# Optimization experiments

Measured on AMD Instinct MI355X. Metric: run time of the kernel, lower is better.

Reference implementation:

```python
import jax, jax.numpy as jnp
import numpy as np

B, T, N = 64, 1024, 1024  # n = 2*hidden_size

def setup_inputs() -> dict:
    key = jax.random.key(0)
    ks = jax.random.split(key, 8)
    s = 1.0 / np.sqrt(N)
    return {
        "s_t_hat": jax.random.normal(ks[0], (B, N), jnp.float32),
        "h": jax.random.normal(ks[1], (B, T, N), jnp.float32),
        "enc_padding_mask": jnp.ones((B, T), jnp.float32),
        "coverage": jax.random.uniform(ks[2], (B, T), jnp.float32),
        "W_h": jax.random.normal(ks[3], (N, N), jnp.float32) * s,   # Linear(N,N,bias=False), [out,in]
        "W_c": jax.random.normal(ks[4], (N,), jnp.float32) * s,     # Linear(1,N,bias=False) weight[:,0]
        "dec_W": jax.random.normal(ks[5], (N, N), jnp.float32) * s, # decode_proj weight [out,in]
        "dec_b": jax.random.normal(ks[6], (N,), jnp.float32) * s,   # decode_proj bias
        "v": jax.random.normal(ks[7], (N,), jnp.float32) * s,       # Linear(N,1,bias=False) weight[0,:]
    }

def reference(s_t_hat, h, enc_padding_mask, coverage, W_h, W_c, dec_W, dec_b, v):
    # encoder_feature = W_h(h): [B,T,N]
    enc_feat = jnp.einsum("btn,mn->btm", h, W_h)
    # dec_fea = decode_proj(s_t_hat): [B,N], broadcast over T
    dec_fea = s_t_hat @ dec_W.T + dec_b
    att = enc_feat + dec_fea[:, None, :]
    # coverage feature: coverage[...,None] * W_c row (Linear(1,N))
    att = att + coverage[:, :, None] * W_c[None, None, :]
    # scores = v(tanh(att)): [B,T]
    scores = jnp.einsum("btn,n->bt", jnp.tanh(att), v)
    attn_ = jax.nn.softmax(scores, axis=1) * enc_padding_mask
    attn = attn_ / jnp.sum(attn_, axis=1, keepdims=True)
    # context vector: [B,N]
    c_t = jnp.einsum("bt,btn->bn", attn, h)
    coverage_new = coverage + attn
    return (c_t, attn, coverage_new)
```

## Files before the change

kernel.cpp:

```cpp
#include <hip/hip_runtime.h>

typedef __bf16 bf16x8 __attribute__((ext_vector_type(8)));
typedef float f32x4 __attribute__((ext_vector_type(4)));
typedef unsigned short us8 __attribute__((ext_vector_type(8)));

#define B_ 64
#define T_ 1024
#define N_ 1024

__device__ __forceinline__ unsigned short f2bf(float f) {
  unsigned int u = __float_as_uint(f);
  u += 0x7fffu + ((u >> 16) & 1u);
  return (unsigned short)(u >> 16);
}

__device__ __forceinline__ float fast_tanh(float x) {
  float xc = fminf(fmaxf(x, -15.f), 15.f);
  float e = __expf(2.f * xc);
  return (e - 1.f) / (e + 1.f);
}

__device__ __forceinline__ void async16(const unsigned short* g, unsigned short* l) {
  __builtin_amdgcn_global_load_lds((const __attribute__((address_space(1))) void*)g,
                                   (__attribute__((address_space(3))) void*)l, 16, 0, 0);
}

__global__ __launch_bounds__(256) void k_cvt_wh(const float* __restrict__ W_h,
                                                unsigned short* __restrict__ whb,
                                                float* __restrict__ scores,
                                                float* __restrict__ ct) {
  int base = blockIdx.x * 256 + threadIdx.x;
  size_t i = (size_t)base * 4;
  float4 x = *(const float4*)(W_h + i);
  ushort4 o;
  o.x = f2bf(x.x); o.y = f2bf(x.y); o.z = f2bf(x.z); o.w = f2bf(x.w);
  *(ushort4*)(whb + i) = o;
  if (base < B_ * T_) scores[base] = 0.f;
  if (base < B_ * N_) ct[base] = 0.f;
}

__global__ __launch_bounds__(256) void k_cvt_h(const float* __restrict__ h,
                                               unsigned short* __restrict__ hbf) {
  size_t i = ((size_t)blockIdx.x * 256 + threadIdx.x) * 8;
  float4 x = *(const float4*)(h + i);
  float4 y = *(const float4*)(h + i + 4);
  us8 o;
  o[0] = f2bf(x.x); o[1] = f2bf(x.y); o[2] = f2bf(x.z); o[3] = f2bf(x.w);
  o[4] = f2bf(y.x); o[5] = f2bf(y.y); o[6] = f2bf(y.z); o[7] = f2bf(y.w);
  *(us8*)(hbf + i) = o;
}

__global__ __launch_bounds__(256) void k_decfea2(const float* __restrict__ s_t_hat,
                                                 const float* __restrict__ dec_W,
                                                 const float* __restrict__ dec_b,
                                                 float* __restrict__ dec_fea) {
  const int m0 = blockIdx.x * 64;
  const int bg0 = blockIdx.y * 8;
  __shared__ float sh[8][N_];
  __shared__ float red[4][64][8];
  const int tid = threadIdx.x;
  for (int idx = tid; idx < 8 * N_; idx += 256) {
    int bb = idx >> 10, k = idx & (N_ - 1);
    sh[bb][k] = s_t_hat[(size_t)(bg0 + bb) * N_ + k];
  }
  __syncthreads();
  const int tm = tid >> 2;
  const int seg = tid & 3;
  const float* w = dec_W + (size_t)(m0 + tm) * N_;
  float acc[8];
#pragma unroll
  for (int bb = 0; bb < 8; bb++) acc[bb] = 0.f;
  for (int i = 0; i < 64; i++) {
    int k = seg * 4 + i * 16;
    float4 wv = *(const float4*)(w + k);
#pragma unroll
    for (int bb = 0; bb < 8; bb++)
      acc[bb] += sh[bb][k] * wv.x + sh[bb][k + 1] * wv.y + sh[bb][k + 2] * wv.z + sh[bb][k + 3] * wv.w;
  }
#pragma unroll
  for (int bb = 0; bb < 8; bb++) red[seg][tm][bb] = acc[bb];
  __syncthreads();
  int om = tid & 63, ob = tid >> 6;
#pragma unroll
  for (int p = 0; p < 2; p++) {
    int obb = ob + p * 4;
    float s = red[0][om][obb] + red[1][om][obb] + red[2][om][obb] + red[3][om][obb] + dec_b[m0 + om];
    dec_fea[(size_t)(bg0 + obb) * N_ + m0 + om] = s;
  }
}

__global__ __launch_bounds__(256) void k_score2(
    const unsigned short* __restrict__ hbf, const unsigned short* __restrict__ whb,
    const float* __restrict__ dec_fea, const float* __restrict__ coverage,
    const float* __restrict__ W_c, const float* __restrict__ v,
    float* __restrict__ scores) {
  __shared__ __align__(16) unsigned short lsA[128 * 32];
  __shared__ __align__(16) unsigned short lsB[128 * 32];

  const int tid = threadIdx.x;
  const int bid = blockIdx.x;
  const int xcd = bid & 7;
  const int local = bid >> 3;
  const int mi = local & 7;
  const int tb = xcd * 64 + (local >> 3);
  const int b = tb >> 3;
  const int t0 = (tb & 7) * 128;
  const int m0 = mi * 128;

  const int wave = tid >> 6, lane = tid & 63;
  const int wr = wave >> 1, wc = wave & 1;
  const int lm = lane & 15, lq = lane >> 4;

  f32x4 acc[4][4];
#pragma unroll
  for (int i = 0; i < 4; i++)
#pragma unroll
    for (int j = 0; j < 4; j++) acc[i][j] = (f32x4){0.f, 0.f, 0.f, 0.f};

  const int r0 = tid >> 2;
  const int key0 = (r0 & 3) ^ ((r0 >> 2) & 3);
  const int cc = ((tid & 3) ^ key0) * 8;
  const unsigned short* gA = hbf + ((size_t)(b * T_ + t0)) * N_;
  const unsigned short* gB = whb + (size_t)m0 * N_;
  const size_t ga0 = (size_t)r0 * N_ + cc;
  const size_t ga1 = (size_t)(r0 + 64) * N_ + cc;
  unsigned short* la0 = &lsA[tid * 8];
  unsigned short* la1 = &lsA[(tid + 256) * 8];
  unsigned short* lb0 = &lsB[tid * 8];
  unsigned short* lb1 = &lsB[(tid + 256) * 8];

  const int keyL = (lm & 3) ^ ((lm >> 2) & 3);
  const int rdoff = (lq ^ keyL) * 8;

  for (int k0 = 0; k0 < N_; k0 += 32) {
    async16(gA + ga0 + k0, la0);
    async16(gA + ga1 + k0, la1);
    async16(gB + ga0 + k0, lb0);
    async16(gB + ga1 + k0, lb1);
    __syncthreads();

    bf16x8 af[4], bfr[4];
#pragma unroll
    for (int i = 0; i < 4; i++)
      af[i] = __builtin_bit_cast(bf16x8, *(const us8*)&lsA[(wr * 64 + i * 16 + lm) * 32 + rdoff]);
#pragma unroll
    for (int j = 0; j < 4; j++)
      bfr[j] = __builtin_bit_cast(bf16x8, *(const us8*)&lsB[(wc * 64 + j * 16 + lm) * 32 + rdoff]);
#pragma unroll
    for (int i = 0; i < 4; i++)
#pragma unroll
      for (int j = 0; j < 4; j++)
        acc[i][j] = __builtin_amdgcn_mfma_f32_16x16x32_bf16(af[i], bfr[j], acc[i][j], 0, 0, 0);
    __syncthreads();
  }

  float dfv[4], wcv[4], vv[4];
#pragma unroll
  for (int j = 0; j < 4; j++) {
    int m = m0 + wc * 64 + j * 16 + lm;
    dfv[j] = dec_fea[b * N_ + m];
    wcv[j] = W_c[m];
    vv[j] = v[m];
  }
#pragma unroll
  for (int i = 0; i < 4; i++) {
#pragma unroll
    for (int r = 0; r < 4; r++) {
      int t = t0 + wr * 64 + i * 16 + lq * 4 + r;
      float cv = coverage[b * T_ + t];
      float s = 0.f;
#pragma unroll
      for (int j = 0; j < 4; j++) {
        float x = acc[i][j][r] + dfv[j] + cv * wcv[j];
        s += fast_tanh(x) * vv[j];
      }
      s += __shfl_xor(s, 1);
      s += __shfl_xor(s, 2);
      s += __shfl_xor(s, 4);
      s += __shfl_xor(s, 8);
      if (lm == 0) atomicAdd(&scores[b * T_ + t], s);
    }
  }
}

__global__ __launch_bounds__(256) void k_score_fb(
    const float* __restrict__ h, const unsigned short* __restrict__ whb,
    const float* __restrict__ dec_fea, const float* __restrict__ coverage,
    const float* __restrict__ W_c, const float* __restrict__ v,
    float* __restrict__ scores) {
  __shared__ __align__(16) unsigned short lsA[128 * 40];
  __shared__ __align__(16) unsigned short lsB[128 * 40];
  const int tid = threadIdx.x;
  const int b = blockIdx.z;
  const int t0 = blockIdx.y * 128;
  const int m0 = blockIdx.x * 128;
  const int wave = tid >> 6, lane = tid & 63;
  const int wr = wave >> 1, wc = wave & 1;
  const int lm = lane & 15, lq = lane >> 4;
  f32x4 acc[4][4];
#pragma unroll
  for (int i = 0; i < 4; i++)
#pragma unroll
    for (int j = 0; j < 4; j++) acc[i][j] = (f32x4){0.f, 0.f, 0.f, 0.f};
  const float* hA = h + ((size_t)b * T_ + t0) * N_;
  const unsigned short* wB = whb + (size_t)m0 * N_;
  for (int k0 = 0; k0 < N_; k0 += 32) {
    __syncthreads();
    for (int s = tid; s < 512; s += 256) {
      int row = s >> 2, kc = (s & 3) * 8;
      const float* src = hA + (size_t)row * N_ + k0 + kc;
      float4 x = *(const float4*)src;
      float4 y = *(const float4*)(src + 4);
      unsigned short* d = &lsA[row * 40 + kc];
      d[0] = f2bf(x.x); d[1] = f2bf(x.y); d[2] = f2bf(x.z); d[3] = f2bf(x.w);
      d[4] = f2bf(y.x); d[5] = f2bf(y.y); d[6] = f2bf(y.z); d[7] = f2bf(y.w);
    }
    for (int s = tid; s < 512; s += 256) {
      int row = s >> 2, kc = (s & 3) * 8;
      us8 x = *(const us8*)(wB + (size_t)row * N_ + k0 + kc);
      *(us8*)&lsB[row * 40 + kc] = x;
    }
    __syncthreads();
    bf16x8 af[4], bfr[4];
#pragma unroll
    for (int i = 0; i < 4; i++)
      af[i] = __builtin_bit_cast(bf16x8, *(const us8*)&lsA[(wr * 64 + i * 16 + lm) * 40 + lq * 8]);
#pragma unroll
    for (int j = 0; j < 4; j++)
      bfr[j] = __builtin_bit_cast(bf16x8, *(const us8*)&lsB[(wc * 64 + j * 16 + lm) * 40 + lq * 8]);
#pragma unroll
    for (int i = 0; i < 4; i++)
#pragma unroll
      for (int j = 0; j < 4; j++)
        acc[i][j] = __builtin_amdgcn_mfma_f32_16x16x32_bf16(af[i], bfr[j], acc[i][j], 0, 0, 0);
  }
  float dfv[4], wcv[4], vv[4];
#pragma unroll
  for (int j = 0; j < 4; j++) {
    int m = m0 + wc * 64 + j * 16 + lm;
    dfv[j] = dec_fea[b * N_ + m];
    wcv[j] = W_c[m];
    vv[j] = v[m];
  }
#pragma unroll
  for (int i = 0; i < 4; i++) {
#pragma unroll
    for (int r = 0; r < 4; r++) {
      int t = t0 + wr * 64 + i * 16 + lq * 4 + r;
      float cv = coverage[b * T_ + t];
      float s = 0.f;
#pragma unroll
      for (int j = 0; j < 4; j++) {
        float x = acc[i][j][r] + dfv[j] + cv * wcv[j];
        s += fast_tanh(x) * vv[j];
      }
      s += __shfl_xor(s, 1);
      s += __shfl_xor(s, 2);
      s += __shfl_xor(s, 4);
      s += __shfl_xor(s, 8);
      if (lm == 0) atomicAdd(&scores[b * T_ + t], s);
    }
  }
}

__global__ __launch_bounds__(256) void k_softmax(const float* __restrict__ scores,
                                                 const float* __restrict__ mask,
                                                 const float* __restrict__ coverage,
                                                 float* __restrict__ attn_out,
                                                 float* __restrict__ cov_out) {
  const int b = blockIdx.x, tid = threadIdx.x;
  const int wave = tid >> 6, lane = tid & 63;
  const float* s = scores + b * T_;
  float vals[4];
  float lmax = -1e30f;
#pragma unroll
  for (int i = 0; i < 4; i++) {
    vals[i] = s[i * 256 + tid];
    lmax = fmaxf(lmax, vals[i]);
  }
#pragma unroll
  for (int off = 1; off < 64; off <<= 1) lmax = fmaxf(lmax, __shfl_xor(lmax, off));
  __shared__ float rmax[4], rsum[4];
  if (lane == 0) rmax[wave] = lmax;
  __syncthreads();
  float bmax = fmaxf(fmaxf(rmax[0], rmax[1]), fmaxf(rmax[2], rmax[3]));
  float w[4];
  float lsum = 0.f;
#pragma unroll
  for (int i = 0; i < 4; i++) {
    float e = __expf(vals[i] - bmax) * mask[b * T_ + i * 256 + tid];
    w[i] = e;
    lsum += e;
  }
#pragma unroll
  for (int off = 1; off < 64; off <<= 1) lsum += __shfl_xor(lsum, off);
  if (lane == 0) rsum[wave] = lsum;
  __syncthreads();
  float inv = 1.f / (rsum[0] + rsum[1] + rsum[2] + rsum[3]);
#pragma unroll
  for (int i = 0; i < 4; i++) {
    int t = i * 256 + tid;
    float a = w[i] * inv;
    attn_out[b * T_ + t] = a;
    cov_out[b * T_ + t] = coverage[b * T_ + t] + a;
  }
}

__global__ __launch_bounds__(256) void k_ctx2(const unsigned short* __restrict__ hbf,
                                              const float* __restrict__ attn,
                                              float* __restrict__ c_t) {
  const int b = blockIdx.y;
  const int t0 = blockIdx.x * 128;
  const int tid = threadIdx.x;
  const int n0 = (tid & 127) * 8;
  const int tp = tid >> 7;
  __shared__ float la[128];
  __shared__ float part[128][8];
  if (tid < 128) la[tid] = attn[b * T_ + t0 + tid];
  __syncthreads();
  float acc[8] = {0.f, 0.f, 0.f, 0.f, 0.f, 0.f, 0.f, 0.f};
  for (int t = tp; t < 128; t += 2) {
    const uint4 u = *(const uint4*)(hbf + ((size_t)(b * T_ + t0 + t)) * N_ + n0);
    float a = la[t];
    acc[0] += a * __uint_as_float(u.x << 16);
    acc[1] += a * __uint_as_float(u.x & 0xffff0000u);
    acc[2] += a * __uint_as_float(u.y << 16);
    acc[3] += a * __uint_as_float(u.y & 0xffff0000u);
    acc[4] += a * __uint_as_float(u.z << 16);
    acc[5] += a * __uint_as_float(u.z & 0xffff0000u);
    acc[6] += a * __uint_as_float(u.w << 16);
    acc[7] += a * __uint_as_float(u.w & 0xffff0000u);
  }
  if (tp == 1) {
#pragma unroll
    for (int j = 0; j < 8; j++) part[tid & 127][j] = acc[j];
  }
  __syncthreads();
  if (tp == 0) {
#pragma unroll
    for (int j = 0; j < 8; j++)
      atomicAdd(&c_t[b * N_ + n0 + j], acc[j] + part[tid][j]);
  }
}

__global__ __launch_bounds__(256) void k_ctx_fb(const float* __restrict__ h,
                                                const float* __restrict__ attn,
                                                float* __restrict__ c_t) {
  const int b = blockIdx.y;
  const int n = blockIdx.x * 256 + threadIdx.x;
  __shared__ float la[T_];
  for (int i = threadIdx.x; i < T_; i += 256) la[i] = attn[b * T_ + i];
  __syncthreads();
  const float* hb = h + (size_t)b * T_ * N_ + n;
  float acc = 0.f;
#pragma unroll 8
  for (int t = 0; t < T_; t++) acc += la[t] * hb[(size_t)t * N_];
  c_t[b * N_ + n] = acc;
}

extern "C" void kernel_launch(void* const* d_in, const int* in_sizes, int n_in,
                              void* d_out, int out_size, void* d_ws, size_t ws_size,
                              hipStream_t stream) {
  const float* s_t_hat  = (const float*)d_in[0];
  const float* h        = (const float*)d_in[1];
  const float* mask     = (const float*)d_in[2];
  const float* coverage = (const float*)d_in[3];
  const float* W_h      = (const float*)d_in[4];
  const float* W_c      = (const float*)d_in[5];
  const float* dec_W    = (const float*)d_in[6];
  const float* dec_b    = (const float*)d_in[7];
  const float* v        = (const float*)d_in[8];

  float* out = (float*)d_out;
  float* out_ct   = out;
  float* out_attn = out + B_ * T_;
  float* out_cov  = out + 2 * B_ * T_;

  const size_t hbf_bytes = (size_t)B_ * T_ * N_ * 2;
  const size_t whb_bytes = (size_t)N_ * N_ * 2;
  const size_t df_bytes  = (size_t)B_ * N_ * 4;
  const size_t sc_bytes  = (size_t)B_ * T_ * 4;
  const bool big = ws_size >= hbf_bytes + whb_bytes + df_bytes + sc_bytes;

  char* ws = (char*)d_ws;
  if (big) {
    unsigned short* hbf = (unsigned short*)ws;
    unsigned short* whb = (unsigned short*)(ws + hbf_bytes);
    float* dec_fea = (float*)(ws + hbf_bytes + whb_bytes);
    float* scores  = (float*)(ws + hbf_bytes + whb_bytes + df_bytes);

    k_cvt_wh<<<dim3(N_ * N_ / 1024), 256, 0, stream>>>(W_h, whb, scores, out_ct);
    k_cvt_h<<<dim3(B_ * T_ * N_ / 2048), 256, 0, stream>>>(h, hbf);
    k_decfea2<<<dim3(16, 8), 256, 0, stream>>>(s_t_hat, dec_W, dec_b, dec_fea);
    k_score2<<<dim3(4096), 256, 0, stream>>>(hbf, whb, dec_fea, coverage, W_c, v, scores);
    k_softmax<<<dim3(B_), 256, 0, stream>>>(scores, mask, coverage, out_attn, out_cov);
    k_ctx2<<<dim3(T_ / 128, B_), 256, 0, stream>>>(hbf, out_attn, out_ct);
  } else {
    unsigned short* whb = (unsigned short*)ws;
    float* dec_fea = (float*)(ws + whb_bytes);
    float* scores  = (float*)(ws + whb_bytes + df_bytes);

    k_cvt_wh<<<dim3(N_ * N_ / 1024), 256, 0, stream>>>(W_h, whb, scores, out_ct);
    k_decfea2<<<dim3(16, 8), 256, 0, stream>>>(s_t_hat, dec_W, dec_b, dec_fea);
    k_score_fb<<<dim3(N_ / 128, T_ / 128, B_), 256, 0, stream>>>(h, whb, dec_fea, coverage, W_c, v, scores);
    k_softmax<<<dim3(B_), 256, 0, stream>>>(scores, mask, coverage, out_attn, out_cov);
    k_ctx_fb<<<dim3(4, B_), 256, 0, stream>>>(h, out_attn, out_ct);
  }
}
```

Measured before the change: 672.0 us.

## Pre-swizzle h and W_h into MFMA fragment layout, drop LDS staging

The bf16 conversion kernels now write h and W_h in a tiled layout where each 16x32 tile is stored in the exact per-lane order the MFMA fragment expects. The score GEMM then loads fragments straight from global memory into registers with double buffering, removing the LDS async copies and the two barriers per k-step. The context kernel is rewritten to read the same swizzled layout, reducing across lanes with shuffles before the atomics. The risk is that tiles in a block are no longer reused through LDS, so the GEMM leans on L2 for reuse and global load latency is less well hidden.

```diff
diff --git a/kernel.cpp b/kernel.cpp
--- a/kernel.cpp
+++ b/kernel.cpp
@@ -20,34 +20,44 @@
   return (e - 1.f) / (e + 1.f);
 }
 
-__device__ __forceinline__ void async16(const unsigned short* g, unsigned short* l) {
-  __builtin_amdgcn_global_load_lds((const __attribute__((address_space(1))) void*)g,
-                                   (__attribute__((address_space(3))) void*)l, 16, 0, 0);
-}
-
-__global__ __launch_bounds__(256) void k_cvt_wh(const float* __restrict__ W_h,
-                                                unsigned short* __restrict__ whb,
-                                                float* __restrict__ scores,
-                                                float* __restrict__ ct) {
-  int base = blockIdx.x * 256 + threadIdx.x;
-  size_t i = (size_t)base * 4;
-  float4 x = *(const float4*)(W_h + i);
-  ushort4 o;
-  o.x = f2bf(x.x); o.y = f2bf(x.y); o.z = f2bf(x.z); o.w = f2bf(x.w);
-  *(ushort4*)(whb + i) = o;
-  if (base < B_ * T_) scores[base] = 0.f;
-  if (base < B_ * N_) ct[base] = 0.f;
-}
-
-__global__ __launch_bounds__(256) void k_cvt_h(const float* __restrict__ h,
-                                               unsigned short* __restrict__ hbf) {
-  size_t i = ((size_t)blockIdx.x * 256 + threadIdx.x) * 8;
-  float4 x = *(const float4*)(h + i);
-  float4 y = *(const float4*)(h + i + 4);
+
+__global__ __launch_bounds__(256) void k_swz_w(const float* __restrict__ W_h,
+                                               unsigned short* __restrict__ wsw,
+                                               float* __restrict__ scores,
+                                               float* __restrict__ ct) {
+  const int tau = blockIdx.x * 4 + (threadIdx.x >> 6);
+  const int l = threadIdx.x & 63;
+  const int mb = tau >> 5, kb = tau & 31;
+  const int row = mb * 16 + (l & 15);
+  const int kof = kb * 32 + (l >> 4) * 8;
+  const float* src = W_h + (size_t)row * N_ + kof;
+  float4 x = *(const float4*)src;
+  float4 y = *(const float4*)(src + 4);
   us8 o;
   o[0] = f2bf(x.x); o[1] = f2bf(x.y); o[2] = f2bf(x.z); o[3] = f2bf(x.w);
   o[4] = f2bf(y.x); o[5] = f2bf(y.y); o[6] = f2bf(y.z); o[7] = f2bf(y.w);
-  *(us8*)(hbf + i) = o;
+  *(us8*)(wsw + (size_t)tau * 512 + l * 8) = o;
+  const int gid = blockIdx.x * 256 + threadIdx.x;
+  if (gid < B_ * T_) scores[gid] = 0.f;
+  if (gid < B_ * N_) ct[gid] = 0.f;
+}
+
+__global__ __launch_bounds__(256) void k_swz_h(const float* __restrict__ h,
+                                               unsigned short* __restrict__ hs) {
+  const int tau = blockIdx.x * 4 + (threadIdx.x >> 6);
+  const int l = threadIdx.x & 63;
+  const int b = tau >> 11;
+  const int tb = (tau >> 5) & 63;
+  const int kb = tau & 31;
+  const int row = tb * 16 + (l & 15);
+  const int kof = kb * 32 + (l >> 4) * 8;
+  const float* src = h + ((size_t)(b << 10) + row) * N_ + kof;
+  float4 x = *(const float4*)src;
+  float4 y = *(const float4*)(src + 4);
+  us8 o;
+  o[0] = f2bf(x.x); o[1] = f2bf(x.y); o[2] = f2bf(x.z); o[3] = f2bf(x.w);
+  o[4] = f2bf(y.x); o[5] = f2bf(y.y); o[6] = f2bf(y.z); o[7] = f2bf(y.w);
+  *(us8*)(hs + (size_t)tau * 512 + l * 8) = o;
 }
 
 __global__ __launch_bounds__(256) void k_decfea2(const float* __restrict__ s_t_hat,
@@ -89,14 +99,11 @@
   }
 }
 
-__global__ __launch_bounds__(256) void k_score2(
-    const unsigned short* __restrict__ hbf, const unsigned short* __restrict__ whb,
+__global__ __launch_bounds__(256) void k_score3(
+    const unsigned short* __restrict__ hs, const unsigned short* __restrict__ wsw,
     const float* __restrict__ dec_fea, const float* __restrict__ coverage,
     const float* __restrict__ W_c, const float* __restrict__ v,
     float* __restrict__ scores) {
-  __shared__ __align__(16) unsigned short lsA[128 * 32];
-  __shared__ __align__(16) unsigned short lsB[128 * 32];
-
   const int tid = threadIdx.x;
   const int bid = blockIdx.x;
   const int xcd = bid & 7;
@@ -104,8 +111,9 @@
   const int mi = local & 7;
   const int tb = xcd * 64 + (local >> 3);
   const int b = tb >> 3;
-  const int t0 = (tb & 7) * 128;
+  const int t8 = tb & 7;
   const int m0 = mi * 128;
+  const int t0 = t8 * 128;
 
   const int wave = tid >> 6, lane = tid & 63;
   const int wr = wave >> 1, wc = wave & 1;
@@ -117,41 +125,42 @@
 #pragma unroll
     for (int j = 0; j < 4; j++) acc[i][j] = (f32x4){0.f, 0.f, 0.f, 0.f};
 
-  const int r0 = tid >> 2;
-  const int key0 = (r0 & 3) ^ ((r0 >> 2) & 3);
-  const int cc = ((tid & 3) ^ key0) * 8;
-  const unsigned short* gA = hbf + ((size_t)(b * T_ + t0)) * N_;
-  const unsigned short* gB = whb + (size_t)m0 * N_;
-  const size_t ga0 = (size_t)r0 * N_ + cc;
-  const size_t ga1 = (size_t)(r0 + 64) * N_ + cc;
-  unsigned short* la0 = &lsA[tid * 8];
-  unsigned short* la1 = &lsA[(tid + 256) * 8];
-  unsigned short* lb0 = &lsB[tid * 8];
-  unsigned short* lb1 = &lsB[(tid + 256) * 8];
-
-  const int keyL = (lm & 3) ^ ((lm >> 2) & 3);
-  const int rdoff = (lq ^ keyL) * 8;
-
-  for (int k0 = 0; k0 < N_; k0 += 32) {
-    async16(gA + ga0 + k0, la0);
-    async16(gA + ga1 + k0, la1);
-    async16(gB + ga0 + k0, lb0);
-    async16(gB + ga1 + k0, lb1);
-    __syncthreads();
-
-    bf16x8 af[4], bfr[4];
+  const unsigned short* pA = hs + (((size_t)b * 64 + t8 * 8 + wr * 4) << 5 << 9) + lane * 8;
+  const unsigned short* pB = wsw + (((size_t)(mi * 8 + wc * 4)) << 5 << 9) + lane * 8;
+
+  us8 aA[4], bA[4], aB[4], bB[4];
+#pragma unroll
+  for (int i = 0; i < 4; i++) {
+    aA[i] = *(const us8*)(pA + ((i << 5) << 9));
+    bA[i] = *(const us8*)(pB + ((i << 5) << 9));
+  }
+  for (int kb = 0; kb < 32; kb += 2) {
+#pragma unroll
+    for (int i = 0; i < 4; i++) {
+      aB[i] = *(const us8*)(pA + (((i << 5) + kb + 1) << 9));
+      bB[i] = *(const us8*)(pB + (((i << 5) + kb + 1) << 9));
+    }
 #pragma unroll
     for (int i = 0; i < 4; i++)
-      af[i] = __builtin_bit_cast(bf16x8, *(const us8*)&lsA[(wr * 64 + i * 16 + lm) * 32 + rdoff]);
-#pragma unroll
-    for (int j = 0; j < 4; j++)
-      bfr[j] = __builtin_bit_cast(bf16x8, *(const us8*)&lsB[(wc * 64 + j * 16 + lm) * 32 + rdoff]);
+#pragma unroll
+      for (int j = 0; j < 4; j++)
+        acc[i][j] = __builtin_amdgcn_mfma_f32_16x16x32_bf16(
+            __builtin_bit_cast(bf16x8, aA[i]), __builtin_bit_cast(bf16x8, bA[j]),
+            acc[i][j], 0, 0, 0);
+    if (kb + 2 < 32) {
+#pragma unroll
+      for (int i = 0; i < 4; i++) {
+        aA[i] = *(const us8*)(pA + (((i << 5) + kb + 2) << 9));
+        bA[i] = *(const us8*)(pB + (((i << 5) + kb + 2) << 9));
+      }
+    }
 #pragma unroll
     for (int i = 0; i < 4; i++)
 #pragma unroll
       for (int j = 0; j < 4; j++)
-        acc[i][j] = __builtin_amdgcn_mfma_f32_16x16x32_bf16(af[i], bfr[j], acc[i][j], 0, 0, 0);
-    __syncthreads();
+        acc[i][j] = __builtin_amdgcn_mfma_f32_16x16x32_bf16(
+            __builtin_bit_cast(bf16x8, aB[i]), __builtin_bit_cast(bf16x8, bB[j]),
+            acc[i][j], 0, 0, 0);
   }
 
   float dfv[4], wcv[4], vv[4];
@@ -263,6 +272,20 @@
   }
 }
 
+__global__ __launch_bounds__(256) void k_cvt_wh(const float* __restrict__ W_h,
+                                                unsigned short* __restrict__ whb,
+                                                float* __restrict__ scores,
+                                                float* __restrict__ ct) {
+  int base = blockIdx.x * 256 + threadIdx.x;
+  size_t i = (size_t)base * 4;
+  float4 x = *(const float4*)(W_h + i);
+  ushort4 o;
+  o.x = f2bf(x.x); o.y = f2bf(x.y); o.z = f2bf(x.z); o.w = f2bf(x.w);
+  *(ushort4*)(whb + i) = o;
+  if (base < B_ * T_) scores[base] = 0.f;
+  if (base < B_ * N_) ct[base] = 0.f;
+}
+
 __global__ __launch_bounds__(256) void k_softmax(const float* __restrict__ scores,
                                                  const float* __restrict__ mask,
                                                  const float* __restrict__ coverage,
@@ -306,40 +329,37 @@
   }
 }
 
-__global__ __launch_bounds__(256) void k_ctx2(const unsigned short* __restrict__ hbf,
+__global__ __launch_bounds__(256) void k_ctx3(const unsigned short* __restrict__ hs,
                                               const float* __restrict__ attn,
                                               float* __restrict__ c_t) {
   const int b = blockIdx.y;
-  const int t0 = blockIdx.x * 128;
-  const int tid = threadIdx.x;
-  const int n0 = (tid & 127) * 8;
-  const int tp = tid >> 7;
-  __shared__ float la[128];
-  __shared__ float part[128][8];
-  if (tid < 128) la[tid] = attn[b * T_ + t0 + tid];
-  __syncthreads();
+  const int z = blockIdx.z;
+  const int kb = blockIdx.x * 4 + (threadIdx.x >> 6);
+  const int l = threadIdx.x & 63;
+  __shared__ float la[T_];
+  for (int i = threadIdx.x; i < T_; i += 256) la[i] = attn[b * T_ + i];
+  __syncthreads();
+  const unsigned short* p = hs + (((size_t)b * 64 + z * 32) << 5 << 9) + ((size_t)kb << 9) + l * 8;
   float acc[8] = {0.f, 0.f, 0.f, 0.f, 0.f, 0.f, 0.f, 0.f};
-  for (int t = tp; t < 128; t += 2) {
-    const uint4 u = *(const uint4*)(hbf + ((size_t)(b * T_ + t0 + t)) * N_ + n0);
-    float a = la[t];
-    acc[0] += a * __uint_as_float(u.x << 16);
-    acc[1] += a * __uint_as_float(u.x & 0xffff0000u);
-    acc[2] += a * __uint_as_float(u.y << 16);
-    acc[3] += a * __uint_as_float(u.y & 0xffff0000u);
-    acc[4] += a * __uint_as_float(u.z << 16);
-    acc[5] += a * __uint_as_float(u.z & 0xffff0000u);
-    acc[6] += a * __uint_as_float(u.w << 16);
-    acc[7] += a * __uint_as_float(u.w & 0xffff0000u);
-  }
-  if (tp == 1) {
-#pragma unroll
-    for (int j = 0; j < 8; j++) part[tid & 127][j] = acc[j];
-  }
-  __syncthreads();
-  if (tp == 0) {
-#pragma unroll
-    for (int j = 0; j < 8; j++)
-      atomicAdd(&c_t[b * N_ + n0 + j], acc[j] + part[tid][j]);
+  const int trow = l & 15;
+#pragma unroll 4
+  for (int tb = 0; tb < 32; tb++) {
+    us8 u = *(const us8*)(p + ((size_t)tb << 5 << 9));
+    float a = la[(z * 32 + tb) * 16 + trow];
+#pragma unroll
+    for (int j = 0; j < 8; j++) acc[j] += a * __uint_as_float((unsigned)u[j] << 16);
+  }
+#pragma unroll
+  for (int j = 0; j < 8; j++) {
+    acc[j] += __shfl_xor(acc[j], 1);
+    acc[j] += __shfl_xor(acc[j], 2);
+    acc[j] += __shfl_xor(acc[j], 4);
+    acc[j] += __shfl_xor(acc[j], 8);
+  }
+  if (trow == 0) {
+    int n0 = kb * 32 + (l >> 4) * 8;
+#pragma unroll
+    for (int j = 0; j < 8; j++) atomicAdd(&c_t[b * N_ + n0 + j], acc[j]);
   }
 }
 
@@ -384,17 +404,17 @@
 
   char* ws = (char*)d_ws;
   if (big) {
-    unsigned short* hbf = (unsigned short*)ws;
-    unsigned short* whb = (unsigned short*)(ws + hbf_bytes);
+    unsigned short* hs  = (unsigned short*)ws;
+    unsigned short* wsw = (unsigned short*)(ws + hbf_bytes);
     float* dec_fea = (float*)(ws + hbf_bytes + whb_bytes);
     float* scores  = (float*)(ws + hbf_bytes + whb_bytes + df_bytes);
 
-    k_cvt_wh<<<dim3(N_ * N_ / 1024), 256, 0, stream>>>(W_h, whb, scores, out_ct);
-    k_cvt_h<<<dim3(B_ * T_ * N_ / 2048), 256, 0, stream>>>(h, hbf);
+    k_swz_w<<<dim3(512), 256, 0, stream>>>(W_h, wsw, scores, out_ct);
+    k_swz_h<<<dim3(32768), 256, 0, stream>>>(h, hs);
     k_decfea2<<<dim3(16, 8), 256, 0, stream>>>(s_t_hat, dec_W, dec_b, dec_fea);
-    k_score2<<<dim3(4096), 256, 0, stream>>>(hbf, whb, dec_fea, coverage, W_c, v, scores);
+    k_score3<<<dim3(4096), 256, 0, stream>>>(hs, wsw, dec_fea, coverage, W_c, v, scores);
     k_softmax<<<dim3(B_), 256, 0, stream>>>(scores, mask, coverage, out_attn, out_cov);
-    k_ctx2<<<dim3(T_ / 128, B_), 256, 0, stream>>>(hbf, out_attn, out_ct);
+    k_ctx3<<<dim3(8, B_, 2), 256, 0, stream>>>(hs, out_attn, out_ct);
   } else {
     unsigned short* whb = (unsigned short*)ws;
     float* dec_fea = (float*)(ws + whb_bytes);
```

Result: no change. 675.6 us (+0.5%).
